# Optimization experiments

Measured on AMD Instinct MI355X. Metric: run time of the kernel, lower is better.

## Reference

```python
import jax, jax.numpy as jnp
import numpy as np

E = 8          # num_global_experts (experts['count_per_node'])
D = 1024       # model_dim
H = 2048       # expert hidden_size
TOP_K = 2      # gate_type['k']


def setup_inputs() -> dict:
    key = jax.random.key(0)
    k_x, k_g, k_w1, k_w2 = jax.random.split(key, 4)
    B, S = 4, 2048
    inp = {
        "input": jax.random.normal(k_x, (B, S, D), dtype=jnp.float32),
        "Wg": jax.random.normal(k_g, (D, E), dtype=jnp.float32) * 0.02,
        "W1": jax.random.normal(k_w1, (E, D, H), dtype=jnp.float32) * 0.02,
        "b1": jnp.zeros((E, H), dtype=jnp.float32),
        "W2": jax.random.normal(k_w2, (E, H, D), dtype=jnp.float32) * 0.02,
        "b2": jnp.zeros((E, D), dtype=jnp.float32),
    }
    return inp


def reference(input, Wg, W1, b1, W2, b2):
    # ---- router: top-k softmax gating, gate weights normalized over top-k ----
    logits = jnp.einsum("bsd,de->bse", input, Wg)            # [B,S,E]
    probs = jax.nn.softmax(logits, axis=-1)                   # [B,S,E]
    top_vals, top_idx = jax.lax.top_k(probs, TOP_K)           # [B,S,K]
    top_vals = top_vals / jnp.sum(top_vals, axis=-1, keepdims=True)
    onehot = jax.nn.one_hot(top_idx, E, dtype=input.dtype)    # [B,S,K,E]
    mask = jnp.sum(onehot, axis=2)                            # [B,S,E] 0/1 dispatch mask (indices)
    scores = jnp.sum(onehot * top_vals[..., None], axis=2)    # [B,S,E] combine weights

    # ---- dense masked dispatch: repeat input per expert, mask non-routed tokens ----
    xm = input[None] * jnp.moveaxis(mask, -1, 0)[..., None]   # [E,B,S,D]

    # ---- per-expert 2-layer MLP (LinearExperts) ----
    h = jnp.einsum("ebsd,edh->ebsh", xm, W1) + b1[:, None, None, :]
    h = jax.nn.relu(h)                                        # [E,B,S,H]
    y = jnp.einsum("ebsh,ehd->ebsd", h, W2) + b2[:, None, None, :]

    # ---- weighted combine: sum_e expert_out * gate score ----
    out = jnp.sum(y * jnp.moveaxis(scores, -1, 0)[..., None], axis=0)  # [B,S,D]
    return out
```

## Files before the change

### kernel.cpp

```cpp
#include <hip/hip_runtime.h>
#include <hip/hip_bf16.h>

typedef __bf16 bf16x8 __attribute__((ext_vector_type(8)));
typedef __bf16 bf16x4 __attribute__((ext_vector_type(4)));
typedef float  f32x4  __attribute__((ext_vector_type(4)));

#define T_TOK    8192
#define D_DIM    1024
#define H_DIM    2048
#define E_NUM    8
#define MAX_ROWS 17408
#define MAX_MB256 72

#define OFF_MBTOT   512
#define OFF_MB2E    1024
#define OFF_MBROW0  2048
#define OFF_MBEND   3072
#define OFF_TOPKE   4096
#define OFF_TOPKS   69632
#define OFF_TOK     135168
#define OFF_ROWIDX  204800
#define OFF_XB      (1u<<20)
#define OFF_W1T     (18u*1024*1024)
#define OFF_W2T     (50u*1024*1024)
#define OFF_HBUF    (82u*1024*1024)
#define OFF_YBUF    OFF_XB

__device__ __forceinline__ void gload_lds16(const void* g, void* l) {
    __builtin_amdgcn_global_load_lds(
        (const __attribute__((address_space(1))) void*)g,
        (__attribute__((address_space(3))) void*)l, 16, 0, 0);
}

__global__ __launch_bounds__(256) void k_router_cvt(
    const float* __restrict__ x, const float* __restrict__ Wg,
    __bf16* __restrict__ xb, int* __restrict__ topk_e, float* __restrict__ topk_s)
{
    __shared__ float wgT[E_NUM][1032];
    const int tid = threadIdx.x;
#pragma unroll
    for (int i = 0; i < 32; ++i) {
        int f = tid + i * 256;
        wgT[f & 7][f >> 3] = Wg[f];
    }
    __syncthreads();

    const int wave = tid >> 6, lane = tid & 63;
    const int t = blockIdx.x * 4 + wave;
    const float* xr = x + (size_t)t * D_DIM;
    __bf16* xbr = xb + (size_t)t * D_DIM;

    float acc[E_NUM];
#pragma unroll
    for (int e = 0; e < E_NUM; ++e) acc[e] = 0.f;

#pragma unroll
    for (int j = 0; j < 4; ++j) {
        const int d0 = lane * 4 + j * 256;
        float4 xv = *(const float4*)(xr + d0);
        bf16x4 o = { (__bf16)xv.x, (__bf16)xv.y, (__bf16)xv.z, (__bf16)xv.w };
        *(bf16x4*)(xbr + d0) = o;
#pragma unroll
        for (int e = 0; e < E_NUM; ++e) {
            float4 wv = *(const float4*)&wgT[e][d0];
            acc[e] += xv.x * wv.x + xv.y * wv.y + xv.z * wv.z + xv.w * wv.w;
        }
    }
#pragma unroll
    for (int off = 32; off >= 1; off >>= 1)
#pragma unroll
        for (int e = 0; e < E_NUM; ++e) acc[e] += __shfl_xor(acc[e], off, 64);

    if (lane == 0) {
        int e0 = 0; float v0 = acc[0];
#pragma unroll
        for (int e = 1; e < E_NUM; ++e) if (acc[e] > v0) { v0 = acc[e]; e0 = e; }
        int e1 = -1; float v1 = -1e30f;
#pragma unroll
        for (int e = 0; e < E_NUM; ++e) if (e != e0 && acc[e] > v1) { v1 = acc[e]; e1 = e; }
        float s0 = 1.f / (1.f + __expf(v1 - v0));
        float s1 = 1.f - s0;
        topk_e[t*2+0] = e0; topk_e[t*2+1] = e1;
        topk_s[t*2+0] = s0; topk_s[t*2+1] = s1;
    }
}

#define SORT_T 256
__global__ __launch_bounds__(512) void k_sort(
    const int* __restrict__ topk_e,
    int* __restrict__ mbTot, int* __restrict__ mb2e, int* __restrict__ mbrow0,
    int* __restrict__ mbrowEnd, int* __restrict__ tok, int* __restrict__ rowidx)
{
    __shared__ int lcnt[E_NUM][SORT_T];
    __shared__ int base[E_NUM];
    __shared__ int etot[E_NUM];
    const int tid = threadIdx.x;

    if (tid < SORT_T) {
#pragma unroll
        for (int e = 0; e < E_NUM; ++e) lcnt[e][tid] = 0;
    }
    __syncthreads();

    if (tid < SORT_T) {
        const int4* p = (const int4*)(topk_e + tid * 64);
#pragma unroll
        for (int i = 0; i < 16; ++i) {
            int4 v = p[i];
            lcnt[v.x][tid]++; lcnt[v.y][tid]++; lcnt[v.z][tid]++; lcnt[v.w][tid]++;
        }
    }
    __syncthreads();

    {
        const int w = tid >> 6, l = tid & 63;
        int v0 = lcnt[w][l*4+0], v1 = lcnt[w][l*4+1], v2 = lcnt[w][l*4+2], v3 = lcnt[w][l*4+3];
        int s = v0 + v1 + v2 + v3;
        int inc = s;
#pragma unroll
        for (int off = 1; off < 64; off <<= 1) {
            int o = __shfl_up(inc, off, 64);
            if (l >= off) inc += o;
        }
        int exc = inc - s;
        lcnt[w][l*4+0] = exc;
        lcnt[w][l*4+1] = exc + v0;
        lcnt[w][l*4+2] = exc + v0 + v1;
        lcnt[w][l*4+3] = exc + v0 + v1 + v2;
        if (l == 63) etot[w] = inc;
    }
    __syncthreads();

    if (tid == 0) {
        int row = 0, mb = 0;
        for (int e = 0; e < E_NUM; ++e) {
            base[e] = row;
            int nb128 = (etot[e] + 127) >> 7;
            int len   = nb128 << 7;
            int nb    = (nb128 + 1) >> 1;
            for (int b = 0; b < nb; ++b) {
                mb2e[mb]   = e;
                mbrow0[mb] = row + b * 256;
                int re = row + len, be = row + b * 256 + 256;
                mbrowEnd[mb] = re < be ? re : be;
                ++mb;
            }
            row += len;
        }
        mbTot[0] = mb;
        mbTot[1] = row;
    }
    __syncthreads();

    if (tid < SORT_T) {
#pragma unroll
        for (int e = 0; e < E_NUM; ++e) lcnt[e][tid] += base[e];
        const int4* p = (const int4*)(topk_e + tid * 64);
#pragma unroll
        for (int i = 0; i < 16; ++i) {
            int4 v = p[i];
            int j0 = tid * 64 + i * 4;
            int r;
            r = lcnt[v.x][tid]++; tok[r] = (j0+0) >> 1; rowidx[j0+0] = r;
            r = lcnt[v.y][tid]++; tok[r] = (j0+1) >> 1; rowidx[j0+1] = r;
            r = lcnt[v.z][tid]++; tok[r] = (j0+2) >> 1; rowidx[j0+2] = r;
            r = lcnt[v.w][tid]++; tok[r] = (j0+3) >> 1; rowidx[j0+3] = r;
        }
    }
}

__global__ __launch_bounds__(256) void k_transpose(
    const float* __restrict__ in, __bf16* __restrict__ out, int R, int C)
{
    __shared__ float tile[64][65];
    const int e = blockIdx.z;
    const float* inp = in + (size_t)e * R * C;
    __bf16* outp = out + (size_t)e * R * C;
    const int r0 = blockIdx.x * 64, c0 = blockIdx.y * 64;
    const int c = threadIdx.x & 63, rr = threadIdx.x >> 6;
#pragma unroll
    for (int i = 0; i < 16; ++i) {
        int r = rr + i * 4;
        tile[r][c] = inp[(size_t)(r0 + r) * C + c0 + c];
    }
    __syncthreads();
#pragma unroll
    for (int i = 0; i < 16; ++i) {
        int cc = rr + i * 4;
        outp[(size_t)(c0 + cc) * R + r0 + c] = (__bf16)tile[c][cc];
    }
}


template<int BUF, int MIB>
__device__ __forceinline__ void rd_av(const char* sm, int wm, int r, int q, bf16x8 (&av)[4][2]) {
    const int rx = r & 7;
    const char* ab = sm + BUF*32768 + wm*16384 + r*128;
#pragma unroll
    for (int m2 = 0; m2 < 4; ++m2) {
        const char* rp = ab + (MIB*64 + m2*16)*128;
        av[m2][0] = *(const bf16x8*)(rp + (((0|q) ^ rx) << 4));
        av[m2][1] = *(const bf16x8*)(rp + (((4|q) ^ rx) << 4));
    }
}
template<int BUF, int NIB>
__device__ __forceinline__ void rd_bv(const char* sm, int wn, int r, int q, bf16x8 (&bv)[2][2][2]) {
    const int rx = r & 7;
    const char* bb = sm + 65536 + BUF*32768 + (wn>>1)*16384 + ((wn&1)*64 + NIB*32 + r)*128;
#pragma unroll
    for (int n2 = 0; n2 < 2; ++n2) {
        const char* rp = bb + n2*16*128;
        bv[NIB][n2][0] = *(const bf16x8*)(rp + (((0|q) ^ rx) << 4));
        bv[NIB][n2][1] = *(const bf16x8*)(rp + (((4|q) ^ rx) << 4));
    }
}
template<int MIB, int NIB>
__device__ __forceinline__ void mfma16(const bf16x8 (&av)[4][2], const bf16x8 (&bv)[2][2][2],
                                       f32x4 (&acc)[8][4]) {
#pragma unroll
    for (int m2 = 0; m2 < 4; ++m2)
#pragma unroll
        for (int n2 = 0; n2 < 2; ++n2) {
            f32x4 c = acc[MIB*4+m2][NIB*2+n2];
            c = __builtin_amdgcn_mfma_f32_16x16x32_bf16(av[m2][0], bv[NIB][n2][0], c, 0, 0, 0);
            c = __builtin_amdgcn_mfma_f32_16x16x32_bf16(av[m2][1], bv[NIB][n2][1], c, 0, 0, 0);
            acc[MIB*4+m2][NIB*2+n2] = c;
        }
}

#define BARR __builtin_amdgcn_s_barrier()
#define WLG  asm volatile("s_waitcnt lgkmcnt(0)" ::: "memory")
#define WLG8 asm volatile("s_waitcnt lgkmcnt(8)" ::: "memory")
#define WVM4 asm volatile("s_waitcnt vmcnt(4)" ::: "memory")
#define WVM0 asm volatile("s_waitcnt vmcnt(0)" ::: "memory")
#define P1 __builtin_amdgcn_s_setprio(1)
#define P0 __builtin_amdgcn_s_setprio(0)
#define STAGE_A(B_, H_, T_) { \
    gload_lds16(pA[H_][0] + (T_)*64, smem + (B_)*32768 + (H_)*16384 + wq); \
    gload_lds16(pA[H_][1] + (T_)*64, smem + (B_)*32768 + (H_)*16384 + 8192 + wq); }
#define STAGE_B(B_, H_, T_) { \
    gload_lds16(pB[H_][0] + (T_)*64, smem + 65536 + (B_)*32768 + (H_)*16384 + wq); \
    gload_lds16(pB[H_][1] + (T_)*64, smem + 65536 + (B_)*32768 + (H_)*16384 + 8192 + wq); }

template<int KD, int NBLK, bool GATHER, bool RELU>
__global__ __launch_bounds__(512, 2) void k_gemm8(
    const __bf16* __restrict__ Asrc, const __bf16* __restrict__ WT,
    const float* __restrict__ bias, const int* __restrict__ tok,
    const int* __restrict__ mb2e, const int* __restrict__ mbrow0,
    const int* __restrict__ mbrowEnd, const int* __restrict__ mbTot,
    __bf16* __restrict__ outp)
{
    constexpr int NT = KD / 64;
    constexpr int NOUT = NBLK * 256;
    __shared__ __align__(16) char smem[131072];

    const int id   = blockIdx.x;
    const int xcd  = id & 7;
    const int j    = id >> 3;
    const int nblk = j % NBLK;
    const int mbi  = (j / NBLK) * 8 + xcd;
    if (mbi >= mbTot[0]) return;
    const int rowTot = mbTot[1];
    const int e    = mb2e[mbi];
    const int row0 = mbrow0[mbi];
    const int rEnd = mbrowEnd[mbi];
    const int n0   = nblk * 256;

    const int tid = threadIdx.x;
    const int w = tid >> 6, l = tid & 63;
    const int r = l & 15, q = l >> 4;
    const int wm = w >> 2, wn = w & 3;
    const int wq = w * 1024;

    const int Rrow = l >> 3;
    const int cg   = (l & 7) ^ Rrow;
    const __bf16* Wb = WT + (size_t)e * ((size_t)NOUT * KD);
    const __bf16* pA[2][2]; const __bf16* pB[2][2];
#pragma unroll
    for (int h = 0; h < 2; ++h)
#pragma unroll
        for (int s = 0; s < 2; ++s) {
            int R  = s*64 + w*8 + Rrow;
            int ra = row0 + h*128 + R;
            ra = ra < rowTot ? ra : (rowTot - 1);
            if (GATHER) pA[h][s] = Asrc + (size_t)tok[ra] * KD + cg*8;
            else        pA[h][s] = Asrc + (size_t)ra * KD + cg*8;
            pB[h][s] = Wb + (size_t)(n0 + h*128 + R) * KD + cg*8;
        }

    f32x4 acc[8][4];
#pragma unroll
    for (int mi = 0; mi < 8; ++mi)
#pragma unroll
        for (int ni = 0; ni < 4; ++ni) acc[mi][ni] = (f32x4){0.f, 0.f, 0.f, 0.f};

    bf16x8 av[4][2];
    bf16x8 bv[2][2][2];

    STAGE_B(0,0,0); STAGE_B(0,1,0); STAGE_A(0,0,0); STAGE_A(0,1,0);
    STAGE_B(1,0,1); STAGE_B(1,1,1);
    WVM4; BARR;

    for (int t0 = 0; t0 < NT - 2; t0 += 2) {
        rd_av<0,0>(smem, wm, r, q, av); rd_bv<0,0>(smem, wn, r, q, bv);
        STAGE_A(1,0,t0+1);
        WLG8; BARR; WLG; P1; mfma16<0,0>(av, bv, acc); P0; BARR;
        rd_bv<0,1>(smem, wn, r, q, bv);
        STAGE_A(1,1,t0+1);
        BARR; WLG; P1; mfma16<0,1>(av, bv, acc); P0; BARR;
        rd_av<0,1>(smem, wm, r, q, av);
        STAGE_B(0,0,t0+2);
        BARR; WLG; P1; mfma16<1,0>(av, bv, acc); P0; BARR;
        STAGE_B(0,1,t0+2);
        BARR; WLG; P1; mfma16<1,1>(av, bv, acc); P0; WVM4; BARR;
        rd_av<1,0>(smem, wm, r, q, av); rd_bv<1,0>(smem, wn, r, q, bv);
        STAGE_A(0,0,t0+2);
        WLG8; BARR; WLG; P1; mfma16<0,0>(av, bv, acc); P0; BARR;
        rd_bv<1,1>(smem, wn, r, q, bv);
        STAGE_A(0,1,t0+2);
        BARR; WLG; P1; mfma16<0,1>(av, bv, acc); P0; BARR;
        rd_av<1,1>(smem, wm, r, q, av);
        STAGE_B(1,0,t0+3);
        BARR; WLG; P1; mfma16<1,0>(av, bv, acc); P0; BARR;
        STAGE_B(1,1,t0+3);
        BARR; WLG; P1; mfma16<1,1>(av, bv, acc); P0; WVM4; BARR;
    }
    {
        const int t0 = NT - 2;
        rd_av<0,0>(smem, wm, r, q, av); rd_bv<0,0>(smem, wn, r, q, bv);
        STAGE_A(1,0,t0+1);
        WLG8; BARR; WLG; P1; mfma16<0,0>(av, bv, acc); P0; BARR;
        rd_bv<0,1>(smem, wn, r, q, bv);
        STAGE_A(1,1,t0+1);
        BARR; WLG; P1; mfma16<0,1>(av, bv, acc); P0; BARR;
        rd_av<0,1>(smem, wm, r, q, av);
        BARR; WLG; P1; mfma16<1,0>(av, bv, acc); P0; BARR;
        BARR; WLG; P1; mfma16<1,1>(av, bv, acc); P0; WVM0; BARR;
        rd_av<1,0>(smem, wm, r, q, av); rd_bv<1,0>(smem, wn, r, q, bv);
        BARR; WLG; P1; mfma16<0,0>(av, bv, acc); P0; BARR;
        rd_bv<1,1>(smem, wn, r, q, bv);
        BARR; WLG; P1; mfma16<0,1>(av, bv, acc); P0; BARR;
        rd_av<1,1>(smem, wm, r, q, av);
        BARR; WLG; P1; mfma16<1,0>(av, bv, acc); P0; BARR;
        BARR; WLG; P1; mfma16<1,1>(av, bv, acc); P0; BARR;
    }

    const float* be = bias + (size_t)e * NOUT;
    float bb4[4];
#pragma unroll
    for (int n2 = 0; n2 < 4; ++n2) bb4[n2] = be[n0 + wn*64 + n2*16 + r];
#pragma unroll
    for (int mi = 0; mi < 8; ++mi)
#pragma unroll
        for (int reg = 0; reg < 4; ++reg) {
            int row = row0 + wm*128 + mi*16 + q*4 + reg;
            if (row < rEnd) {
                __bf16* orow = outp + (size_t)row * NOUT + n0 + wn*64;
#pragma unroll
                for (int n2 = 0; n2 < 4; ++n2) {
                    float v = acc[mi][n2][reg] + bb4[n2];
                    if (RELU) v = fmaxf(v, 0.f);
                    orow[n2*16 + r] = (__bf16)v;
                }
            }
        }
}

__global__ __launch_bounds__(256) void k_combine(
    const __bf16* __restrict__ ybuf, const int* __restrict__ rowidx,
    const float* __restrict__ topk_s, float* __restrict__ out)
{
    const int t = blockIdx.x;
    const int d0 = threadIdx.x * 4;
    const int r0 = rowidx[t*2+0], r1 = rowidx[t*2+1];
    const float s0 = topk_s[t*2+0], s1 = topk_s[t*2+1];
    bf16x4 y0 = *(const bf16x4*)(ybuf + (size_t)r0 * D_DIM + d0);
    bf16x4 y1 = *(const bf16x4*)(ybuf + (size_t)r1 * D_DIM + d0);
    float4 o;
    o.x = s0 * (float)y0[0] + s1 * (float)y1[0];
    o.y = s0 * (float)y0[1] + s1 * (float)y1[1];
    o.z = s0 * (float)y0[2] + s1 * (float)y1[2];
    o.w = s0 * (float)y0[3] + s1 * (float)y1[3];
    *(float4*)(out + (size_t)t * D_DIM + d0) = o;
}

extern "C" void kernel_launch(void* const* d_in, const int* in_sizes, int n_in,
                              void* d_out, int out_size, void* d_ws, size_t ws_size,
                              hipStream_t stream) {
    const float* x  = (const float*)d_in[0];
    const float* Wg = (const float*)d_in[1];
    const float* W1 = (const float*)d_in[2];
    const float* b1 = (const float*)d_in[3];
    const float* W2 = (const float*)d_in[4];
    const float* b2 = (const float*)d_in[5];
    float* out = (float*)d_out;
    char* ws = (char*)d_ws;

    int*   mbTot  = (int*)  (ws + OFF_MBTOT);
    int*   mb2e   = (int*)  (ws + OFF_MB2E);
    int*   mbrow0 = (int*)  (ws + OFF_MBROW0);
    int*   mbrowEnd = (int*)(ws + OFF_MBEND);
    int*   topk_e = (int*)  (ws + OFF_TOPKE);
    float* topk_s = (float*)(ws + OFF_TOPKS);
    int*   tok    = (int*)  (ws + OFF_TOK);
    int*   rowidx = (int*)  (ws + OFF_ROWIDX);
    __bf16* xb   = (__bf16*)(ws + OFF_XB);
    __bf16* W1T  = (__bf16*)(ws + OFF_W1T);
    __bf16* W2T  = (__bf16*)(ws + OFF_W2T);
    __bf16* hbuf = (__bf16*)(ws + OFF_HBUF);
    __bf16* ybuf = (__bf16*)(ws + OFF_YBUF);

    hipMemsetAsync(ws + OFF_TOK, 0, MAX_ROWS * sizeof(int), stream);

    k_router_cvt<<<T_TOK/4, 256, 0, stream>>>(x, Wg, xb, topk_e, topk_s);
    k_sort      <<<1, 512, 0, stream>>>(topk_e, mbTot, mb2e, mbrow0, mbrowEnd, tok, rowidx);
    k_transpose <<<dim3(D_DIM/64, H_DIM/64, E_NUM), 256, 0, stream>>>(W1, W1T, D_DIM, H_DIM);
    k_transpose <<<dim3(H_DIM/64, D_DIM/64, E_NUM), 256, 0, stream>>>(W2, W2T, H_DIM, D_DIM);

    k_gemm8<D_DIM, H_DIM/256, true,  true ><<<MAX_MB256 * (H_DIM/256), 512, 0, stream>>>(
        xb, W1T, b1, tok, mb2e, mbrow0, mbrowEnd, mbTot, hbuf);
    k_gemm8<H_DIM, D_DIM/256, false, false><<<MAX_MB256 * (D_DIM/256), 512, 0, stream>>>(
        hbuf, W2T, b2, tok, mb2e, mbrow0, mbrowEnd, mbTot, ybuf);

    k_combine<<<T_TOK, 256, 0, stream>>>(ybuf, rowidx, topk_s, out);
}
```

Measured before the change: 446.5 us.

## Restructure GEMM main loop to load full tile fragments into registers before staging

Each tile's A and B fragments are now read from LDS into larger register arrays (av[8][2], bv[4][2]) up front. That frees the whole LDS buffer early, so the next-next tile's A and B global-to-LDS loads can be issued into the same buffer during the second half of the MFMAs. The prologue now preloads both buffers fully, and the loop body is expressed as a TILE macro with finer lgkmcnt waits. The change aims to relax LDS/global-load synchronisation and overlap loads with compute better, at the cost of more VGPRs, which could hurt occupancy under launch_bounds(512,2).

```diff
diff --git a/kernel.cpp b/kernel.cpp
--- a/kernel.cpp
+++ b/kernel.cpp
@@ -193,45 +193,46 @@
 
 
 template<int BUF, int MIB>
-__device__ __forceinline__ void rd_av(const char* sm, int wm, int r, int q, bf16x8 (&av)[4][2]) {
+__device__ __forceinline__ void rd_av(const char* sm, int wm, int r, int q, bf16x8 (&av)[8][2]) {
     const int rx = r & 7;
     const char* ab = sm + BUF*32768 + wm*16384 + r*128;
 #pragma unroll
     for (int m2 = 0; m2 < 4; ++m2) {
         const char* rp = ab + (MIB*64 + m2*16)*128;
-        av[m2][0] = *(const bf16x8*)(rp + (((0|q) ^ rx) << 4));
-        av[m2][1] = *(const bf16x8*)(rp + (((4|q) ^ rx) << 4));
+        av[MIB*4+m2][0] = *(const bf16x8*)(rp + (((0|q) ^ rx) << 4));
+        av[MIB*4+m2][1] = *(const bf16x8*)(rp + (((4|q) ^ rx) << 4));
     }
 }
 template<int BUF, int NIB>
-__device__ __forceinline__ void rd_bv(const char* sm, int wn, int r, int q, bf16x8 (&bv)[2][2][2]) {
+__device__ __forceinline__ void rd_bv(const char* sm, int wn, int r, int q, bf16x8 (&bv)[4][2]) {
     const int rx = r & 7;
     const char* bb = sm + 65536 + BUF*32768 + (wn>>1)*16384 + ((wn&1)*64 + NIB*32 + r)*128;
 #pragma unroll
     for (int n2 = 0; n2 < 2; ++n2) {
         const char* rp = bb + n2*16*128;
-        bv[NIB][n2][0] = *(const bf16x8*)(rp + (((0|q) ^ rx) << 4));
-        bv[NIB][n2][1] = *(const bf16x8*)(rp + (((4|q) ^ rx) << 4));
+        bv[NIB*2+n2][0] = *(const bf16x8*)(rp + (((0|q) ^ rx) << 4));
+        bv[NIB*2+n2][1] = *(const bf16x8*)(rp + (((4|q) ^ rx) << 4));
     }
 }
 template<int MIB, int NIB>
-__device__ __forceinline__ void mfma16(const bf16x8 (&av)[4][2], const bf16x8 (&bv)[2][2][2],
+__device__ __forceinline__ void mfma16(const bf16x8 (&av)[8][2], const bf16x8 (&bv)[4][2],
                                        f32x4 (&acc)[8][4]) {
 #pragma unroll
     for (int m2 = 0; m2 < 4; ++m2)
 #pragma unroll
         for (int n2 = 0; n2 < 2; ++n2) {
             f32x4 c = acc[MIB*4+m2][NIB*2+n2];
-            c = __builtin_amdgcn_mfma_f32_16x16x32_bf16(av[m2][0], bv[NIB][n2][0], c, 0, 0, 0);
-            c = __builtin_amdgcn_mfma_f32_16x16x32_bf16(av[m2][1], bv[NIB][n2][1], c, 0, 0, 0);
+            c = __builtin_amdgcn_mfma_f32_16x16x32_bf16(av[MIB*4+m2][0], bv[NIB*2+n2][0], c, 0, 0, 0);
+            c = __builtin_amdgcn_mfma_f32_16x16x32_bf16(av[MIB*4+m2][1], bv[NIB*2+n2][1], c, 0, 0, 0);
             acc[MIB*4+m2][NIB*2+n2] = c;
         }
 }
 
 #define BARR __builtin_amdgcn_s_barrier()
-#define WLG  asm volatile("s_waitcnt lgkmcnt(0)" ::: "memory")
+#define WLG0 asm volatile("s_waitcnt lgkmcnt(0)" ::: "memory")
+#define WLG4 asm volatile("s_waitcnt lgkmcnt(4)" ::: "memory")
 #define WLG8 asm volatile("s_waitcnt lgkmcnt(8)" ::: "memory")
-#define WVM4 asm volatile("s_waitcnt vmcnt(4)" ::: "memory")
+#define WVM8 asm volatile("s_waitcnt vmcnt(8)" ::: "memory")
 #define WVM0 asm volatile("s_waitcnt vmcnt(0)" ::: "memory")
 #define P1 __builtin_amdgcn_s_setprio(1)
 #define P0 __builtin_amdgcn_s_setprio(0)
@@ -241,6 +242,18 @@
 #define STAGE_B(B_, H_, T_) { \
     gload_lds16(pB[H_][0] + (T_)*64, smem + 65536 + (B_)*32768 + (H_)*16384 + wq); \
     gload_lds16(pB[H_][1] + (T_)*64, smem + 65536 + (B_)*32768 + (H_)*16384 + 8192 + wq); }
+
+#define TILE(BUF_, DOST_, ST_, DRAIN_) { \
+    rd_av<BUF_,0>(smem, wm, r, q, av); rd_bv<BUF_,0>(smem, wn, r, q, bv); rd_bv<BUF_,1>(smem, wn, r, q, bv); \
+    BARR; WLG4; P1; mfma16<0,0>(av, bv, acc); P0; BARR; \
+    rd_av<BUF_,1>(smem, wm, r, q, av); \
+    BARR; WLG8; P1; mfma16<0,1>(av, bv, acc); P0; BARR; \
+    WLG0; \
+    if (DOST_) { STAGE_A(BUF_, 0, ST_); STAGE_A(BUF_, 1, ST_); } \
+    BARR; P1; mfma16<1,0>(av, bv, acc); P0; BARR; \
+    if (DOST_) { STAGE_B(BUF_, 0, ST_); STAGE_B(BUF_, 1, ST_); } \
+    BARR; P1; mfma16<1,1>(av, bv, acc); P0; DRAIN_; BARR; \
+}
 
 template<int KD, int NBLK, bool GATHER, bool RELU>
 __global__ __launch_bounds__(512, 2) void k_gemm8(
@@ -294,56 +307,19 @@
 #pragma unroll
         for (int ni = 0; ni < 4; ++ni) acc[mi][ni] = (f32x4){0.f, 0.f, 0.f, 0.f};
 
-    bf16x8 av[4][2];
-    bf16x8 bv[2][2][2];
-
-    STAGE_B(0,0,0); STAGE_B(0,1,0); STAGE_A(0,0,0); STAGE_A(0,1,0);
-    STAGE_B(1,0,1); STAGE_B(1,1,1);
-    WVM4; BARR;
+    bf16x8 av[8][2];
+    bf16x8 bv[4][2];
+
+    STAGE_A(0,0,0); STAGE_A(0,1,0); STAGE_B(0,0,0); STAGE_B(0,1,0);
+    STAGE_A(1,0,1); STAGE_A(1,1,1); STAGE_B(1,0,1); STAGE_B(1,1,1);
+    WVM8; BARR;
 
     for (int t0 = 0; t0 < NT - 2; t0 += 2) {
-        rd_av<0,0>(smem, wm, r, q, av); rd_bv<0,0>(smem, wn, r, q, bv);
-        STAGE_A(1,0,t0+1);
-        WLG8; BARR; WLG; P1; mfma16<0,0>(av, bv, acc); P0; BARR;
-        rd_bv<0,1>(smem, wn, r, q, bv);
-        STAGE_A(1,1,t0+1);
-        BARR; WLG; P1; mfma16<0,1>(av, bv, acc); P0; BARR;
-        rd_av<0,1>(smem, wm, r, q, av);
-        STAGE_B(0,0,t0+2);
-        BARR; WLG; P1; mfma16<1,0>(av, bv, acc); P0; BARR;
-        STAGE_B(0,1,t0+2);
-        BARR; WLG; P1; mfma16<1,1>(av, bv, acc); P0; WVM4; BARR;
-        rd_av<1,0>(smem, wm, r, q, av); rd_bv<1,0>(smem, wn, r, q, bv);
-        STAGE_A(0,0,t0+2);
-        WLG8; BARR; WLG; P1; mfma16<0,0>(av, bv, acc); P0; BARR;
-        rd_bv<1,1>(smem, wn, r, q, bv);
-        STAGE_A(0,1,t0+2);
-        BARR; WLG; P1; mfma16<0,1>(av, bv, acc); P0; BARR;
-        rd_av<1,1>(smem, wm, r, q, av);
-        STAGE_B(1,0,t0+3);
-        BARR; WLG; P1; mfma16<1,0>(av, bv, acc); P0; BARR;
-        STAGE_B(1,1,t0+3);
-        BARR; WLG; P1; mfma16<1,1>(av, bv, acc); P0; WVM4; BARR;
-    }
-    {
-        const int t0 = NT - 2;
-        rd_av<0,0>(smem, wm, r, q, av); rd_bv<0,0>(smem, wn, r, q, bv);
-        STAGE_A(1,0,t0+1);
-        WLG8; BARR; WLG; P1; mfma16<0,0>(av, bv, acc); P0; BARR;
-        rd_bv<0,1>(smem, wn, r, q, bv);
-        STAGE_A(1,1,t0+1);
-        BARR; WLG; P1; mfma16<0,1>(av, bv, acc); P0; BARR;
-        rd_av<0,1>(smem, wm, r, q, av);
-        BARR; WLG; P1; mfma16<1,0>(av, bv, acc); P0; BARR;
-        BARR; WLG; P1; mfma16<1,1>(av, bv, acc); P0; WVM0; BARR;
-        rd_av<1,0>(smem, wm, r, q, av); rd_bv<1,0>(smem, wn, r, q, bv);
-        BARR; WLG; P1; mfma16<0,0>(av, bv, acc); P0; BARR;
-        rd_bv<1,1>(smem, wn, r, q, bv);
-        BARR; WLG; P1; mfma16<0,1>(av, bv, acc); P0; BARR;
-        rd_av<1,1>(smem, wm, r, q, av);
-        BARR; WLG; P1; mfma16<1,0>(av, bv, acc); P0; BARR;
-        BARR; WLG; P1; mfma16<1,1>(av, bv, acc); P0; BARR;
-    }
+        TILE(0, true, t0+2, WVM8);
+        TILE(1, true, t0+3, WVM8);
+    }
+    TILE(0, false, 0, WVM0);
+    TILE(1, false, 0, (void)0);
 
     const float* be = bias + (size_t)e * NOUT;
     float bb4[4];
```

After: 733.4 us. +64.2%, slower.
